# Performance work log

Hardware: AMD Instinct MI355X
Metric: run time of the kernel (lower is better)

## Reference

```python
import jax, jax.numpy as jnp
import numpy as np

LOC, ST, ED = 10000, 168, 10000      # vocab sizes
D_LOC, D_ST, D_ED = 128, 64, 64      # d_model components
D_SUM = D_LOC + D_ST + D_ED
B, S = 64, 128


def _normalized_adj(g):
    # A_hat = D^-1/2 (g + I) D^-1/2, deg = column sums (torch `sum(_A)` sums dim 0)
    a = g + jnp.eye(LOC, dtype=g.dtype)
    deg = a.sum(axis=0)
    d = deg ** -0.5
    return (d[:, None] * a) * d[None, :]


def setup_inputs() -> dict:
    key = jax.random.key(0)
    ks = jax.random.split(key, 8)
    loc = jax.random.randint(ks[0], (B, S), 0, LOC)
    st = jax.random.randint(ks[1], (B, S), 0, ST)
    ed = jax.random.randint(ks[2], (B, S), 0, ED)
    # sparse-ish random binary graph over locations (avg degree ~10)
    g = (jax.random.uniform(ks[3], (LOC, LOC)) < 0.001).astype(jnp.float32)
    A = _normalized_adj(g)
    W_loc = jax.random.normal(ks[4], (LOC, D_LOC), dtype=jnp.float32) * 0.02
    b_loc = jnp.zeros((D_LOC,), dtype=jnp.float32)
    emb_st = jax.random.normal(ks[5], (ST, D_ST), dtype=jnp.float32) * 0.02
    emb_ed = jax.random.normal(ks[6], (ED, D_ED), dtype=jnp.float32) * 0.02
    return {"loc": loc, "st": st, "ed": ed, "A": A, "W_loc": W_loc,
            "b_loc": b_loc, "emb_st": emb_st, "emb_ed": emb_ed}


def reference(loc, st, ed, A, W_loc, b_loc, emb_st, emb_ed):
    # yt = next start-time indices, padded with 0
    yt = jnp.concatenate(
        [st[:, 1:], jnp.zeros((st.shape[0], 1), dtype=st.dtype)], axis=-1)
    # one_hot(loc) @ A  ==  row gather A[loc]  -> [B, S, LOC]
    loc_feat = A[loc]
    # linear + relu: [B,S,LOC] x [LOC,D_LOC]
    res_loc = jax.nn.relu(jnp.einsum('bsn,nd->bsd', loc_feat, W_loc) + b_loc)
    res_st = emb_st[st]
    res_yt = emb_st[yt]
    res_ed = emb_ed[ed]
    res = jnp.concatenate([res_loc, res_st, res_ed], axis=-1)  # [B,S,D_SUM]
    scale = jnp.sqrt(jnp.float32(D_SUM))
    return (res * scale, res_yt)
```

## Files before the change

kernel.cpp:

```cpp
#include <hip/hip_runtime.h>

#define NLOC 10000
#define NST  168
#define NED  10000
#define NTOK 8192
#define SEQ  128
#define DL   128
#define DST  64
#define DED  64
#define DSUM 256
#define MAXNZ 192
#define ROW4 (NLOC/4)


__device__ __forceinline__ int clampi(int v, int hi) {
    return v < 0 ? 0 : (v >= hi ? hi - 1 : v);
}

__global__ __launch_bounds__(256) void fused_kernel(const int* __restrict__ loc_p,
                                                    const int* __restrict__ st_p,
                                                    const int* __restrict__ ed_p,
                                                    const float* __restrict__ A,
                                                    const float* __restrict__ W,
                                                    const float* __restrict__ bias,
                                                    const float* __restrict__ emb_st,
                                                    const float* __restrict__ emb_ed,
                                                    float* __restrict__ out) {
    const int t   = blockIdx.x;
    const int tid = threadIdx.x;
    const int s   = t & (SEQ - 1);
    const int loc_t = clampi(loc_p[t], NLOC);
    const int st_t  = clampi(st_p[t],  NST);
    const int ed_t  = clampi(ed_p[t],  NED);
    const int yt_t  = (s < SEQ - 1) ? clampi(st_p[t + 1], NST) : 0;

    __shared__ float s_val[MAXNZ];
    __shared__ int   s_idx[MAXNZ];
    __shared__ int   s_cnt;
    if (tid == 0) s_cnt = 0;
    __syncthreads();

    const float4* row = (const float4*)(A + (size_t)loc_t * NLOC);
    for (int i = tid; i < ROW4; i += 256) {
        float4 v = row[i];
        if (v.x != 0.f) { int p = atomicAdd(&s_cnt, 1); if (p < MAXNZ) { s_idx[p] = 4*i+0; s_val[p] = v.x; } }
        if (v.y != 0.f) { int p = atomicAdd(&s_cnt, 1); if (p < MAXNZ) { s_idx[p] = 4*i+1; s_val[p] = v.y; } }
        if (v.z != 0.f) { int p = atomicAdd(&s_cnt, 1); if (p < MAXNZ) { s_idx[p] = 4*i+2; s_val[p] = v.z; } }
        if (v.w != 0.f) { int p = atomicAdd(&s_cnt, 1); if (p < MAXNZ) { s_idx[p] = 4*i+3; s_val[p] = v.w; } }
    }
    __syncthreads();
    const int n = min(s_cnt, MAXNZ);

    float* out0 = out + (size_t)t * DSUM;
    float* out1 = out + (size_t)NTOK * DSUM + (size_t)t * DST;

    if (tid < DL) {
        float acc = bias[tid];
        for (int k = 0; k < n; ++k)
            acc = fmaf(s_val[k], W[(size_t)s_idx[k] * DL + tid], acc);
        out0[tid] = fmaxf(acc, 0.f) * 16.0f;
    } else if (tid < DL + DST) {
        const int d = tid - DL;
        out0[tid] = emb_st[(size_t)st_t * DST + d] * 16.0f;
    } else {
        const int d = tid - DL - DST;
        out0[tid] = emb_ed[(size_t)ed_t * DED + d] * 16.0f;
    }
    if (tid < DST)
        out1[tid] = emb_st[(size_t)yt_t * DST + tid];
}

extern "C" void kernel_launch(void* const* d_in, const int* in_sizes, int n_in,
                              void* d_out, int out_size, void* d_ws, size_t ws_size,
                              hipStream_t stream) {
    fused_kernel<<<NTOK, 256, 0, stream>>>((const int*)d_in[0],
                                           (const int*)d_in[1],
                                           (const int*)d_in[2],
                                           (const float*)d_in[3],
                                           (const float*)d_in[4],
                                           (const float*)d_in[5],
                                           (const float*)d_in[6],
                                           (const float*)d_in[7],
                                           (float*)d_out);
}
```

Before: 507.2 us.

## Deduplicate location rows: compute per-unique-row table then gather per token

Marks which location indices appear among the tokens, computes the sparse row × W_loc projection once per unique location into a workspace table, then gathers the table rows per token. The old kernel scanned a full 40KB row of A for every one of the 8192 tokens, even though many share a location. The row scan also skips the nonzero tests when a whole 16-byte vector is zero. It adds a memset and three launches and needs enough workspace, falling back to the fused kernel otherwise.

```diff
diff --git a/kernel.cpp b/kernel.cpp
--- a/kernel.cpp
+++ b/kernel.cpp
@@ -15,6 +15,79 @@
 
 __device__ __forceinline__ int clampi(int v, int hi) {
     return v < 0 ? 0 : (v >= hi ? hi - 1 : v);
+}
+
+__global__ __launch_bounds__(256) void mark_kernel(const int* __restrict__ loc,
+                                                   int* __restrict__ flags) {
+    int t = blockIdx.x * 256 + threadIdx.x;
+    if (t < NTOK) flags[clampi(loc[t], NLOC)] = 1;
+}
+
+__global__ __launch_bounds__(256) void row_kernel(const float* __restrict__ A,
+                                                  const float* __restrict__ W,
+                                                  const float* __restrict__ bias,
+                                                  const int* __restrict__ flags,
+                                                  float* __restrict__ table) {
+    const int r = blockIdx.x;
+    if (!flags[r]) return;
+    __shared__ float s_val[MAXNZ];
+    __shared__ int   s_idx[MAXNZ];
+    __shared__ int   s_cnt;
+    const int tid = threadIdx.x;
+    if (tid == 0) s_cnt = 0;
+    __syncthreads();
+
+    const uint4* row = (const uint4*)(A + (size_t)r * NLOC);
+    for (int i = tid; i < ROW4; i += 256) {
+        uint4 u = row[i];
+        if (u.x | u.y | u.z | u.w) {
+            float4 v = *(const float4*)&u;
+            if (u.x) { int p = atomicAdd(&s_cnt, 1); if (p < MAXNZ) { s_idx[p] = 4*i+0; s_val[p] = v.x; } }
+            if (u.y) { int p = atomicAdd(&s_cnt, 1); if (p < MAXNZ) { s_idx[p] = 4*i+1; s_val[p] = v.y; } }
+            if (u.z) { int p = atomicAdd(&s_cnt, 1); if (p < MAXNZ) { s_idx[p] = 4*i+2; s_val[p] = v.z; } }
+            if (u.w) { int p = atomicAdd(&s_cnt, 1); if (p < MAXNZ) { s_idx[p] = 4*i+3; s_val[p] = v.w; } }
+        }
+    }
+    __syncthreads();
+
+    const int n = min(s_cnt, MAXNZ);
+    if (tid < DL) {
+        float acc = bias[tid];
+        for (int k = 0; k < n; ++k)
+            acc = fmaf(s_val[k], W[(size_t)s_idx[k] * DL + tid], acc);
+        table[(size_t)r * DL + tid] = fmaxf(acc, 0.f) * 16.0f;
+    }
+}
+
+__global__ __launch_bounds__(256) void gather_kernel(const int* __restrict__ loc,
+                                                     const int* __restrict__ st,
+                                                     const int* __restrict__ ed,
+                                                     const float* __restrict__ emb_st,
+                                                     const float* __restrict__ emb_ed,
+                                                     const float* __restrict__ table,
+                                                     float* __restrict__ out) {
+    const int t   = blockIdx.x;
+    const int tid = threadIdx.x;
+    const int s   = t & (SEQ - 1);
+    const int loc_t = clampi(loc[t], NLOC);
+    const int st_t  = clampi(st[t],  NST);
+    const int ed_t  = clampi(ed[t],  NED);
+    const int yt_t  = (s < SEQ - 1) ? clampi(st[t + 1], NST) : 0;
+
+    float* out0 = out + (size_t)t * DSUM;
+    float* out1 = out + (size_t)NTOK * DSUM + (size_t)t * DST;
+
+    if (tid < DL) {
+        out0[tid] = table[(size_t)loc_t * DL + tid];
+    } else if (tid < DL + DST) {
+        const int d = tid - DL;
+        out0[tid] = emb_st[(size_t)st_t * DST + d] * 16.0f;
+    } else {
+        const int d = tid - DL - DST;
+        out0[tid] = emb_ed[(size_t)ed_t * DED + d] * 16.0f;
+    }
+    if (tid < DST)
+        out1[tid] = emb_st[(size_t)yt_t * DST + tid];
 }
 
 __global__ __launch_bounds__(256) void fused_kernel(const int* __restrict__ loc_p,
@@ -40,13 +113,16 @@
     if (tid == 0) s_cnt = 0;
     __syncthreads();
 
-    const float4* row = (const float4*)(A + (size_t)loc_t * NLOC);
+    const uint4* row = (const uint4*)(A + (size_t)loc_t * NLOC);
     for (int i = tid; i < ROW4; i += 256) {
-        float4 v = row[i];
-        if (v.x != 0.f) { int p = atomicAdd(&s_cnt, 1); if (p < MAXNZ) { s_idx[p] = 4*i+0; s_val[p] = v.x; } }
-        if (v.y != 0.f) { int p = atomicAdd(&s_cnt, 1); if (p < MAXNZ) { s_idx[p] = 4*i+1; s_val[p] = v.y; } }
-        if (v.z != 0.f) { int p = atomicAdd(&s_cnt, 1); if (p < MAXNZ) { s_idx[p] = 4*i+2; s_val[p] = v.z; } }
-        if (v.w != 0.f) { int p = atomicAdd(&s_cnt, 1); if (p < MAXNZ) { s_idx[p] = 4*i+3; s_val[p] = v.w; } }
+        uint4 u = row[i];
+        if (u.x | u.y | u.z | u.w) {
+            float4 v = *(const float4*)&u;
+            if (u.x) { int p = atomicAdd(&s_cnt, 1); if (p < MAXNZ) { s_idx[p] = 4*i+0; s_val[p] = v.x; } }
+            if (u.y) { int p = atomicAdd(&s_cnt, 1); if (p < MAXNZ) { s_idx[p] = 4*i+1; s_val[p] = v.y; } }
+            if (u.z) { int p = atomicAdd(&s_cnt, 1); if (p < MAXNZ) { s_idx[p] = 4*i+2; s_val[p] = v.z; } }
+            if (u.w) { int p = atomicAdd(&s_cnt, 1); if (p < MAXNZ) { s_idx[p] = 4*i+3; s_val[p] = v.w; } }
+        }
     }
     __syncthreads();
     const int n = min(s_cnt, MAXNZ);
@@ -73,13 +149,30 @@
 extern "C" void kernel_launch(void* const* d_in, const int* in_sizes, int n_in,
                               void* d_out, int out_size, void* d_ws, size_t ws_size,
                               hipStream_t stream) {
-    fused_kernel<<<NTOK, 256, 0, stream>>>((const int*)d_in[0],
-                                           (const int*)d_in[1],
-                                           (const int*)d_in[2],
-                                           (const float*)d_in[3],
-                                           (const float*)d_in[4],
-                                           (const float*)d_in[5],
-                                           (const float*)d_in[6],
-                                           (const float*)d_in[7],
-                                           (float*)d_out);
+    const int*   loc    = (const int*)  d_in[0];
+    const int*   st     = (const int*)  d_in[1];
+    const int*   ed     = (const int*)  d_in[2];
+    const float* A      = (const float*)d_in[3];
+    const float* W      = (const float*)d_in[4];
+    const float* bias   = (const float*)d_in[5];
+    const float* emb_st = (const float*)d_in[6];
+    const float* emb_ed = (const float*)d_in[7];
+    float*       out    = (float*)d_out;
+
+    const size_t FLAG_BYTES  = NLOC * sizeof(int);
+    const size_t TABLE_OFF   = 65536;
+    const size_t TABLE_BYTES = (size_t)NLOC * DL * sizeof(float);
+    const size_t WS_NEEDED   = TABLE_OFF + TABLE_BYTES;
+
+    if (ws_size >= WS_NEEDED) {
+        int*   flags = (int*)d_ws;
+        float* table = (float*)((char*)d_ws + TABLE_OFF);
+        (void)hipMemsetAsync(flags, 0, FLAG_BYTES, stream);
+        mark_kernel<<<(NTOK + 255) / 256, 256, 0, stream>>>(loc, flags);
+        row_kernel<<<NLOC, 256, 0, stream>>>(A, W, bias, flags, table);
+        gather_kernel<<<NTOK, 256, 0, stream>>>(loc, st, ed, emb_st, emb_ed, table, out);
+    } else {
+        fused_kernel<<<NTOK, 256, 0, stream>>>(loc, st, ed, A, W, bias,
+                                               emb_st, emb_ed, out);
+    }
 }
```

Result: no change. 512.2 us (+1.0%).
